# Kernel tuning notes

Measured on AMD Instinct MI355X. Metric: run time of the kernel, lower is better.

Reference implementation:

```python
import jax, jax.numpy as jnp
import numpy as np

BIG = 1e30  # stand-in for +inf that keeps gradients finite


def setup_inputs() -> dict:
    key = jax.random.key(0)
    B, D, N = 32, 128, 2048
    kx, ky, kl = jax.random.split(key, 3)
    x = jax.random.normal(kx, (B, D, N), dtype=jnp.float32)
    y = jax.random.normal(ky, (B, D, N), dtype=jnp.float32)
    # ragged cardinalities in [N//2, N]; every set nonempty
    lens = jax.random.randint(kl, (B,), N // 2, N + 1)
    mask = jnp.arange(N)[None, :] < lens[:, None]  # [B, N] bool
    return {"x": x, "y": y, "mask": mask}


def reference(x, y, mask):
    # x, y: [B, D, N]; mask: [B, N] bool (shared between x and y, as in original)
    xt = jnp.transpose(x, (0, 2, 1))  # [B, N, D]
    yt = jnp.transpose(y, (0, 2, 1))  # [B, N, D]
    x2 = jnp.sum(xt * xt, axis=-1)    # [B, N]
    y2 = jnp.sum(yt * yt, axis=-1)    # [B, N]
    # pairwise squared L2: [B, N, N], d[b,i,j] = ||x_i - y_j||^2
    d = x2[:, :, None] + y2[:, None, :] - 2.0 * jnp.einsum("bid,bjd->bij", xt, yt)
    m = mask
    # x_dist: for each valid y_j, min over valid x_i; then sum over valid j
    d_row = jnp.where(m[:, :, None], d, BIG)              # mask invalid i
    x_dist = jnp.sum(jnp.where(m, jnp.min(d_row, axis=1), 0.0), axis=1)  # [B]
    # y_dist: for each valid x_i, min over valid y_j; then sum over valid i
    d_col = jnp.where(m[:, None, :], d, BIG)              # mask invalid j
    y_dist = jnp.sum(jnp.where(m, jnp.min(d_col, axis=2), 0.0), axis=1)  # [B]
    return jnp.mean(x_dist + y_dist)
```

## Files before the change

### kernel.cpp

```cpp
#include <hip/hip_runtime.h>
#include <hip/hip_bf16.h>

#define BATCH 32
#define DIM   128
#define NPTS  2048
#define BIGF  1e30f

#define OFF_XT   0ull
#define OFF_YT   16777216ull
#define OFF_XN   33554432ull
#define OFF_YN   (33554432ull + 262144ull)
#define OFF_RMIN (33554432ull + 2ull * 262144ull)
#define OFF_CMIN (33554432ull + 3ull * 262144ull)

typedef __bf16 bf16x8 __attribute__((ext_vector_type(8)));
typedef float  f32x16 __attribute__((ext_vector_type(16)));

#define ZERO16 {0.f,0.f,0.f,0.f,0.f,0.f,0.f,0.f,0.f,0.f,0.f,0.f,0.f,0.f,0.f,0.f}

__device__ __forceinline__ bool mask_is_i32(const void* m) {
  return ((const unsigned char*)m)[1] == 0;
}
__device__ __forceinline__ bool mask_at(const void* m, bool i32, int idx) {
  return i32 ? (((const int*)m)[idx] != 0) : (((const unsigned char*)m)[idx] != 0);
}

__global__ void chamfer_prep(const float* __restrict__ x, const float* __restrict__ y,
                             const void* __restrict__ mask, char* __restrict__ ws,
                             float* __restrict__ out) {
  __shared__ float buf[128 * 132];
  __shared__ float nrm_part[2][128];

  int blk = blockIdx.x;
  int arr = blk >> 9;
  int b   = (blk >> 4) & 31;
  int nt  = blk & 15;
  int n0  = nt << 7;
  int tid = threadIdx.x;

  const float* src = (arr ? y : x) + (size_t)b * DIM * NPTS;

#pragma unroll
  for (int k = 0; k < 16; ++k) {
    int idx = k * 256 + tid;
    int d = idx >> 5, c4 = idx & 31;
    float4 v = *(const float4*)(src + (size_t)d * NPTS + n0 + c4 * 4);
    *(float4*)&buf[d * 132 + c4 * 4] = v;
  }
  __syncthreads();

  int n = tid & 127, half = tid >> 7;
  char* img = ws + (arr ? OFF_YT : OFF_XT) + ((size_t)b * NPTS + n0 + n) * 256;
  float sq = 0.f;
#pragma unroll
  for (int cl = 0; cl < 8; ++cl) {
    unsigned short h[8];
#pragma unroll
    for (int q = 0; q < 8; ++q) {
      int d = half * 64 + cl * 8 + q;
      float v = buf[d * 132 + n];
      __hip_bfloat16 bv = __float2bfloat16(v);
      h[q] = *(unsigned short*)&bv;
      float vb = __bfloat162float(bv);
      sq = fmaf(vb, vb, sq);
    }
    uint4 pk;
    pk.x = h[0] | ((unsigned)h[1] << 16);
    pk.y = h[2] | ((unsigned)h[3] << 16);
    pk.z = h[4] | ((unsigned)h[5] << 16);
    pk.w = h[6] | ((unsigned)h[7] << 16);
    int cg = half * 8 + cl;
    *(uint4*)(img + ((cg ^ (n & 7)) << 4)) = pk;
  }
  nrm_part[half][n] = sq;
  __syncthreads();
  if (half == 0) {
    float tot = nrm_part[0][n] + nrm_part[1][n];
    int row = n0 + n;
    bool i32 = mask_is_i32(mask);
    bool valid = mask_at(mask, i32, b * NPTS + row);
    float* nrm = (float*)(ws + (arr ? OFF_YN : OFF_XN));
    nrm[b * NPTS + row] = valid ? tot : BIGF;
    if (arr) ((unsigned*)(ws + OFF_CMIN))[b * NPTS + row] = __float_as_uint(BIGF);
  }
  if (blk == 0 && tid == 0) out[0] = 0.f;
}

__global__ __launch_bounds__(512, 2)
void chamfer_dist(char* __restrict__ ws) {
  __shared__ unsigned short ys[2][128 * 128];
  __shared__ unsigned colmin_lds[NPTS];

  int blk = blockIdx.x;
  int b  = blk & 31;
  int it = blk >> 5;
  int i0 = it << 8;
  int tid  = threadIdx.x;
  int lane = tid & 63;
  int w    = tid >> 6;
  int qrow = w >> 1, qcol = w & 1;
  int la31 = lane & 31, la5 = lane >> 5;

  const char* xTb = ws + OFF_XT + (size_t)b * NPTS * 256;
  const char* yTb = ws + OFF_YT + (size_t)b * NPTS * 256;
  const float* xng = (const float*)(ws + OFF_XN) + b * NPTS;
  const float* yng = (const float*)(ws + OFF_YN) + b * NPTS;
  float*    rowming = (float*)(ws + OFF_RMIN) + b * NPTS;
  unsigned* colming = (unsigned*)(ws + OFF_CMIN) + b * NPTS;

#pragma unroll
  for (int k = 0; k < NPTS / 512; ++k)
    colmin_lds[k * 512 + tid] = __float_as_uint(BIGF);

  int r0 = i0 + qrow * 64 + la31;
  int swA = (la31 & 7) << 4;
  const char* xrow0 = xTb + (size_t)r0 * 256;
  const char* xrow1 = xrow0 + 32 * 256;
  bf16x8 Areg0[8], Areg1[8];
#pragma unroll
  for (int kc = 0; kc < 8; ++kc) {
    int dbs = (((kc * 2 + la5) << 4)) ^ swA;
    Areg0[kc] = *(const bf16x8*)(xrow0 + dbs);
    Areg1[kc] = *(const bf16x8*)(xrow1 + dbs);
  }

  float xnr[2][16];
#pragma unroll
  for (int fm = 0; fm < 2; ++fm)
#pragma unroll
    for (int r = 0; r < 16; ++r) {
      int row = qrow * 64 + fm * 32 + (r & 3) + ((r >> 2) << 3) + (la5 << 2);
      xnr[fm][r] = xng[i0 + row];
    }
  float rmin[2][16];
#pragma unroll
  for (int fm = 0; fm < 2; ++fm)
#pragma unroll
    for (int r = 0; r < 16; ++r) rmin[fm][r] = BIGF;

#pragma unroll
  for (int k = 0; k < 4; ++k) {
    int idx = k * 512 + tid;
    *(uint4*)((char*)ys[0] + idx * 16) = *(const uint4*)(yTb + (size_t)idx * 16);
  }
  __syncthreads();

  int sw = (la31 & 7) << 4;
  int pcol0 = (qcol * 64 + la31) * 256;
  int pcol1 = pcol0 + 32 * 256;

  for (int jt = 0; jt < 16; ++jt) {
    int cur = jt & 1;
    uint4 stg0, stg1, stg2, stg3;
    if (jt < 15) {
      const char* base = yTb + (size_t)(jt + 1) * 128 * 256;
      stg0 = *(const uint4*)(base + (size_t)(tid)        * 16);
      stg1 = *(const uint4*)(base + (size_t)(512  + tid) * 16);
      stg2 = *(const uint4*)(base + (size_t)(1024 + tid) * 16);
      stg3 = *(const uint4*)(base + (size_t)(1536 + tid) * 16);
    }
    int j0t = jt * 128 + qcol * 64;
    float ynr0 = yng[j0t + la31];
    float ynr1 = yng[j0t + 32 + la31];

    const char* ysb = (const char*)ys[cur];
    f32x16 acc00 = ZERO16, acc01 = ZERO16, acc10 = ZERO16, acc11 = ZERO16;
#pragma unroll
    for (int kc = 0; kc < 8; ++kc) {
      int dbs = ((kc * 2 + la5) << 4) ^ sw;
      bf16x8 b0 = *(const bf16x8*)(ysb + pcol0 + dbs);
      bf16x8 b1 = *(const bf16x8*)(ysb + pcol1 + dbs);
      acc00 = __builtin_amdgcn_mfma_f32_32x32x16_bf16(Areg0[kc], b0, acc00, 0, 0, 0);
      acc01 = __builtin_amdgcn_mfma_f32_32x32x16_bf16(Areg0[kc], b1, acc01, 0, 0, 0);
      acc10 = __builtin_amdgcn_mfma_f32_32x32x16_bf16(Areg1[kc], b0, acc10, 0, 0, 0);
      acc11 = __builtin_amdgcn_mfma_f32_32x32x16_bf16(Areg1[kc], b1, acc11, 0, 0, 0);
    }
    float cm0 = BIGF, cm1 = BIGF;
#pragma unroll
    for (int r = 0; r < 16; ++r) {
      float d;
      d = fmaxf(fmaf(-2.f, acc00[r], xnr[0][r] + ynr0), 0.f);
      rmin[0][r] = fminf(rmin[0][r], d); cm0 = fminf(cm0, d);
      d = fmaxf(fmaf(-2.f, acc01[r], xnr[0][r] + ynr1), 0.f);
      rmin[0][r] = fminf(rmin[0][r], d); cm1 = fminf(cm1, d);
      d = fmaxf(fmaf(-2.f, acc10[r], xnr[1][r] + ynr0), 0.f);
      rmin[1][r] = fminf(rmin[1][r], d); cm0 = fminf(cm0, d);
      d = fmaxf(fmaf(-2.f, acc11[r], xnr[1][r] + ynr1), 0.f);
      rmin[1][r] = fminf(rmin[1][r], d); cm1 = fminf(cm1, d);
    }
    cm0 = fminf(cm0, __shfl_xor(cm0, 32));
    cm1 = fminf(cm1, __shfl_xor(cm1, 32));
    if (lane < 32) {
      atomicMin(&colmin_lds[j0t + la31],      __float_as_uint(cm0));
      atomicMin(&colmin_lds[j0t + 32 + la31], __float_as_uint(cm1));
    }
    if (jt < 15) {
      char* dst = (char*)ys[cur ^ 1];
      *(uint4*)(dst + (size_t)(tid)        * 16) = stg0;
      *(uint4*)(dst + (size_t)(512  + tid) * 16) = stg1;
      *(uint4*)(dst + (size_t)(1024 + tid) * 16) = stg2;
      *(uint4*)(dst + (size_t)(1536 + tid) * 16) = stg3;
    }
    __syncthreads();
  }

  for (int idx = tid; idx < NPTS; idx += 512)
    atomicMin(&colming[idx], colmin_lds[idx]);

#pragma unroll
  for (int fm = 0; fm < 2; ++fm)
#pragma unroll
    for (int r = 0; r < 16; ++r) {
      float v = rmin[fm][r];
      v = fminf(v, __shfl_xor(v, 1));
      v = fminf(v, __shfl_xor(v, 2));
      v = fminf(v, __shfl_xor(v, 4));
      v = fminf(v, __shfl_xor(v, 8));
      v = fminf(v, __shfl_xor(v, 16));
      if (la31 == 0) {
        int row = qrow * 64 + fm * 32 + (r & 3) + ((r >> 2) << 3) + (la5 << 2);
        rowming[i0 + row] = v;
      }
    }
}

__global__ void chamfer_reduce(const char* __restrict__ ws, const void* __restrict__ mask,
                               float* __restrict__ out) {
  __shared__ float red[256];
  int b = blockIdx.x;
  int tid = threadIdx.x;
  bool i32 = mask_is_i32(mask);
  const float*    rowmin = (const float*)(ws + OFF_RMIN) + b * NPTS;
  const unsigned* colmin = (const unsigned*)(ws + OFF_CMIN) + b * NPTS;
  float s = 0.f;
  for (int i = tid; i < NPTS; i += 256) {
    if (mask_at(mask, i32, b * NPTS + i))
      s += rowmin[i] + __uint_as_float(colmin[i]);
  }
  red[tid] = s;
  __syncthreads();
  for (int st = 128; st > 0; st >>= 1) {
    if (tid < st) red[tid] += red[tid + st];
    __syncthreads();
  }
  if (tid == 0) atomicAdd(out, red[0] * (1.f / BATCH));
}

extern "C" void kernel_launch(void* const* d_in, const int* in_sizes, int n_in,
                              void* d_out, int out_size, void* d_ws, size_t ws_size,
                              hipStream_t stream) {
  const float* x = (const float*)d_in[0];
  const float* y = (const float*)d_in[1];
  const void* mask = d_in[2];
  float* out = (float*)d_out;
  char* ws = (char*)d_ws;

  chamfer_prep<<<1024, 256, 0, stream>>>(x, y, mask, ws, out);
  chamfer_dist<<<256, 512, 0, stream>>>(ws);
  chamfer_reduce<<<32, 256, 0, stream>>>(ws, mask, out);
}
```

Baseline: 159.2 us.

## Skip masked tiles, use direct global-to-LDS loads with new bf16 layout

Prep blocks whose first point is masked out now just write sentinel norms, and dist blocks compute the valid length and skip row tiles past it. They also limit column tiles to that length. The bf16 workspace layout changes from swizzled row-major to chunk-major, and Y tiles (256 columns) are staged with global_load_lds async copies instead of register staging. The distance epilogue moves the x-norm add out of the row-min loop, and reduce uses four times as many blocks. Occupancy drops to one block per CU (larger LDS). The chunk-major LDS reads may hit bank conflicts now that the XOR swizzle is gone.

```diff
diff --git a/kernel.cpp b/kernel.cpp
--- a/kernel.cpp
+++ b/kernel.cpp
@@ -4,17 +4,19 @@
 #define BATCH 32
 #define DIM   128
 #define NPTS  2048
+#define NCH   16
 #define BIGF  1e30f
 
 #define OFF_XT   0ull
 #define OFF_YT   16777216ull
 #define OFF_XN   33554432ull
-#define OFF_YN   (33554432ull + 262144ull)
-#define OFF_RMIN (33554432ull + 2ull * 262144ull)
-#define OFF_CMIN (33554432ull + 3ull * 262144ull)
+#define OFF_YN   (OFF_XN + 262144ull)
+#define OFF_RMIN (OFF_XN + 2ull * 262144ull)
+#define OFF_CMIN (OFF_XN + 3ull * 262144ull)
 
 typedef __bf16 bf16x8 __attribute__((ext_vector_type(8)));
 typedef float  f32x16 __attribute__((ext_vector_type(16)));
+typedef unsigned int u32;
 
 #define ZERO16 {0.f,0.f,0.f,0.f,0.f,0.f,0.f,0.f,0.f,0.f,0.f,0.f,0.f,0.f,0.f,0.f}
 
@@ -23,6 +25,12 @@
 }
 __device__ __forceinline__ bool mask_at(const void* m, bool i32, int idx) {
   return i32 ? (((const int*)m)[idx] != 0) : (((const unsigned char*)m)[idx] != 0);
+}
+
+__device__ __forceinline__ void gll16(const void* g, void* l) {
+  __builtin_amdgcn_global_load_lds(
+      (const __attribute__((address_space(1))) u32*)g,
+      (__attribute__((address_space(3))) u32*)l, 16, 0, 0);
 }
 
 __global__ void chamfer_prep(const float* __restrict__ x, const float* __restrict__ y,
@@ -37,28 +45,40 @@
   int nt  = blk & 15;
   int n0  = nt << 7;
   int tid = threadIdx.x;
+  bool i32m = mask_is_i32(mask);
+
+  if (blk == 0 && tid == 0) out[0] = 0.f;
+
+  float*    nrm  = (float*)(ws + (arr ? OFF_YN : OFF_XN));
+  unsigned* cmin = (unsigned*)(ws + OFF_CMIN);
+
+  if (!mask_at(mask, i32m, b * NPTS + n0)) {
+    if (tid < 128) {
+      nrm[b * NPTS + n0 + tid] = BIGF;
+      if (arr) cmin[b * NPTS + n0 + tid] = __float_as_uint(BIGF);
+    }
+    return;
+  }
 
   const float* src = (arr ? y : x) + (size_t)b * DIM * NPTS;
-
 #pragma unroll
   for (int k = 0; k < 16; ++k) {
     int idx = k * 256 + tid;
     int d = idx >> 5, c4 = idx & 31;
-    float4 v = *(const float4*)(src + (size_t)d * NPTS + n0 + c4 * 4);
-    *(float4*)&buf[d * 132 + c4 * 4] = v;
+    *(float4*)&buf[d * 132 + c4 * 4] =
+        *(const float4*)(src + (size_t)d * NPTS + n0 + c4 * 4);
   }
   __syncthreads();
 
   int n = tid & 127, half = tid >> 7;
-  char* img = ws + (arr ? OFF_YT : OFF_XT) + ((size_t)b * NPTS + n0 + n) * 256;
+  char* imgbase = ws + (arr ? OFF_YT : OFF_XT);
   float sq = 0.f;
 #pragma unroll
   for (int cl = 0; cl < 8; ++cl) {
     unsigned short h[8];
 #pragma unroll
     for (int q = 0; q < 8; ++q) {
-      int d = half * 64 + cl * 8 + q;
-      float v = buf[d * 132 + n];
+      float v = buf[(half * 64 + cl * 8 + q) * 132 + n];
       __hip_bfloat16 bv = __float2bfloat16(v);
       h[q] = *(unsigned short*)&bv;
       float vb = __bfloat162float(bv);
@@ -70,141 +90,141 @@
     pk.z = h[4] | ((unsigned)h[5] << 16);
     pk.w = h[6] | ((unsigned)h[7] << 16);
     int cg = half * 8 + cl;
-    *(uint4*)(img + ((cg ^ (n & 7)) << 4)) = pk;
+    *(uint4*)(imgbase + (((size_t)(b * NCH + cg) * NPTS + n0 + n) << 4)) = pk;
   }
   nrm_part[half][n] = sq;
   __syncthreads();
   if (half == 0) {
     float tot = nrm_part[0][n] + nrm_part[1][n];
     int row = n0 + n;
-    bool i32 = mask_is_i32(mask);
-    bool valid = mask_at(mask, i32, b * NPTS + row);
-    float* nrm = (float*)(ws + (arr ? OFF_YN : OFF_XN));
+    bool valid = mask_at(mask, i32m, b * NPTS + row);
     nrm[b * NPTS + row] = valid ? tot : BIGF;
-    if (arr) ((unsigned*)(ws + OFF_CMIN))[b * NPTS + row] = __float_as_uint(BIGF);
-  }
-  if (blk == 0 && tid == 0) out[0] = 0.f;
-}
-
-__global__ __launch_bounds__(512, 2)
-void chamfer_dist(char* __restrict__ ws) {
-  __shared__ unsigned short ys[2][128 * 128];
+    if (arr) cmin[b * NPTS + row] = __float_as_uint(BIGF);
+  }
+}
+
+__global__ __launch_bounds__(512, 1)
+void chamfer_dist(char* __restrict__ ws, const void* __restrict__ mask) {
+  __shared__ __align__(16) char ysl[2][NCH * 256 * 16];
   __shared__ unsigned colmin_lds[NPTS];
+  __shared__ int lred[8];
 
   int blk = blockIdx.x;
   int b  = blk & 31;
   int it = blk >> 5;
   int i0 = it << 8;
-  int tid  = threadIdx.x;
-  int lane = tid & 63;
-  int w    = tid >> 6;
-  int qrow = w >> 1, qcol = w & 1;
-  int la31 = lane & 31, la5 = lane >> 5;
-
-  const char* xTb = ws + OFF_XT + (size_t)b * NPTS * 256;
-  const char* yTb = ws + OFF_YT + (size_t)b * NPTS * 256;
+  int tid = threadIdx.x, lane = tid & 63, w = tid >> 6;
+  int qrow = w >> 1, qcol = w & 1, la31 = lane & 31, la5 = lane >> 5;
+
+  bool i32m = mask_is_i32(mask);
+  int cnt = 0;
+#pragma unroll
+  for (int k = 0; k < 4; ++k)
+    cnt += mask_at(mask, i32m, b * NPTS + k * 512 + tid) ? 1 : 0;
+#pragma unroll
+  for (int s = 1; s < 64; s <<= 1) cnt += __shfl_xor(cnt, s);
+  if (lane == 0) lred[w] = cnt;
+  __syncthreads();
+  int len = 0;
+#pragma unroll
+  for (int k = 0; k < 8; ++k) len += lred[k];
+  if (i0 >= len) return;
+
+  const char* xTb = ws + OFF_XT + ((size_t)b * NCH * NPTS << 4);
+  const char* yTb = ws + OFF_YT + ((size_t)b * NCH * NPTS << 4);
   const float* xng = (const float*)(ws + OFF_XN) + b * NPTS;
   const float* yng = (const float*)(ws + OFF_YN) + b * NPTS;
   float*    rowming = (float*)(ws + OFF_RMIN) + b * NPTS;
   unsigned* colming = (unsigned*)(ws + OFF_CMIN) + b * NPTS;
 
 #pragma unroll
-  for (int k = 0; k < NPTS / 512; ++k)
+  for (int k = 0; k < 4; ++k)
     colmin_lds[k * 512 + tid] = __float_as_uint(BIGF);
 
   int r0 = i0 + qrow * 64 + la31;
-  int swA = (la31 & 7) << 4;
-  const char* xrow0 = xTb + (size_t)r0 * 256;
-  const char* xrow1 = xrow0 + 32 * 256;
   bf16x8 Areg0[8], Areg1[8];
 #pragma unroll
   for (int kc = 0; kc < 8; ++kc) {
-    int dbs = (((kc * 2 + la5) << 4)) ^ swA;
-    Areg0[kc] = *(const bf16x8*)(xrow0 + dbs);
-    Areg1[kc] = *(const bf16x8*)(xrow1 + dbs);
-  }
-
-  float xnr[2][16];
+    int c = kc * 2 + la5;
+    Areg0[kc] = *(const bf16x8*)(xTb + (((size_t)c * NPTS + r0) << 4));
+    Areg1[kc] = *(const bf16x8*)(xTb + (((size_t)c * NPTS + r0 + 32) << 4));
+  }
+
+  float xnr[2][16], rmin[2][16];
 #pragma unroll
   for (int fm = 0; fm < 2; ++fm)
 #pragma unroll
     for (int r = 0; r < 16; ++r) {
       int row = qrow * 64 + fm * 32 + (r & 3) + ((r >> 2) << 3) + (la5 << 2);
       xnr[fm][r] = xng[i0 + row];
-    }
-  float rmin[2][16];
-#pragma unroll
-  for (int fm = 0; fm < 2; ++fm)
-#pragma unroll
-    for (int r = 0; r < 16; ++r) rmin[fm][r] = BIGF;
-
-#pragma unroll
-  for (int k = 0; k < 4; ++k) {
+      rmin[fm][r] = BIGF;
+    }
+
+  int nT = (len + 255) >> 8;
+
+#pragma unroll
+  for (int k = 0; k < 8; ++k) {
     int idx = k * 512 + tid;
-    *(uint4*)((char*)ys[0] + idx * 16) = *(const uint4*)(yTb + (size_t)idx * 16);
-  }
-  __syncthreads();
-
-  int sw = (la31 & 7) << 4;
-  int pcol0 = (qcol * 64 + la31) * 256;
-  int pcol1 = pcol0 + 32 * 256;
-
-  for (int jt = 0; jt < 16; ++jt) {
-    int cur = jt & 1;
-    uint4 stg0, stg1, stg2, stg3;
-    if (jt < 15) {
-      const char* base = yTb + (size_t)(jt + 1) * 128 * 256;
-      stg0 = *(const uint4*)(base + (size_t)(tid)        * 16);
-      stg1 = *(const uint4*)(base + (size_t)(512  + tid) * 16);
-      stg2 = *(const uint4*)(base + (size_t)(1024 + tid) * 16);
-      stg3 = *(const uint4*)(base + (size_t)(1536 + tid) * 16);
-    }
-    int j0t = jt * 128 + qcol * 64;
-    float ynr0 = yng[j0t + la31];
-    float ynr1 = yng[j0t + 32 + la31];
-
-    const char* ysb = (const char*)ys[cur];
-    f32x16 acc00 = ZERO16, acc01 = ZERO16, acc10 = ZERO16, acc11 = ZERO16;
-#pragma unroll
-    for (int kc = 0; kc < 8; ++kc) {
-      int dbs = ((kc * 2 + la5) << 4) ^ sw;
-      bf16x8 b0 = *(const bf16x8*)(ysb + pcol0 + dbs);
-      bf16x8 b1 = *(const bf16x8*)(ysb + pcol1 + dbs);
-      acc00 = __builtin_amdgcn_mfma_f32_32x32x16_bf16(Areg0[kc], b0, acc00, 0, 0, 0);
-      acc01 = __builtin_amdgcn_mfma_f32_32x32x16_bf16(Areg0[kc], b1, acc01, 0, 0, 0);
-      acc10 = __builtin_amdgcn_mfma_f32_32x32x16_bf16(Areg1[kc], b0, acc10, 0, 0, 0);
-      acc11 = __builtin_amdgcn_mfma_f32_32x32x16_bf16(Areg1[kc], b1, acc11, 0, 0, 0);
-    }
-    float cm0 = BIGF, cm1 = BIGF;
-#pragma unroll
-    for (int r = 0; r < 16; ++r) {
-      float d;
-      d = fmaxf(fmaf(-2.f, acc00[r], xnr[0][r] + ynr0), 0.f);
-      rmin[0][r] = fminf(rmin[0][r], d); cm0 = fminf(cm0, d);
-      d = fmaxf(fmaf(-2.f, acc01[r], xnr[0][r] + ynr1), 0.f);
-      rmin[0][r] = fminf(rmin[0][r], d); cm1 = fminf(cm1, d);
-      d = fmaxf(fmaf(-2.f, acc10[r], xnr[1][r] + ynr0), 0.f);
-      rmin[1][r] = fminf(rmin[1][r], d); cm0 = fminf(cm0, d);
-      d = fmaxf(fmaf(-2.f, acc11[r], xnr[1][r] + ynr1), 0.f);
-      rmin[1][r] = fminf(rmin[1][r], d); cm1 = fminf(cm1, d);
-    }
-    cm0 = fminf(cm0, __shfl_xor(cm0, 32));
-    cm1 = fminf(cm1, __shfl_xor(cm1, 32));
-    if (lane < 32) {
-      atomicMin(&colmin_lds[j0t + la31],      __float_as_uint(cm0));
-      atomicMin(&colmin_lds[j0t + 32 + la31], __float_as_uint(cm1));
-    }
-    if (jt < 15) {
-      char* dst = (char*)ys[cur ^ 1];
-      *(uint4*)(dst + (size_t)(tid)        * 16) = stg0;
-      *(uint4*)(dst + (size_t)(512  + tid) * 16) = stg1;
-      *(uint4*)(dst + (size_t)(1024 + tid) * 16) = stg2;
-      *(uint4*)(dst + (size_t)(1536 + tid) * 16) = stg3;
+    gll16(yTb + (((size_t)(idx >> 8) * NPTS + (idx & 255)) << 4),
+          &ysl[0][idx * 16]);
+  }
+  __syncthreads();
+
+  for (int t = 0; t < nT; ++t) {
+    int cur = t & 1;
+    if (t + 1 < nT) {
+      int j0n = (t + 1) << 8;
+#pragma unroll
+      for (int k = 0; k < 8; ++k) {
+        int idx = k * 512 + tid;
+        gll16(yTb + (((size_t)(idx >> 8) * NPTS + j0n + (idx & 255)) << 4),
+              &ysl[cur ^ 1][idx * 16]);
+      }
+    }
+    const char* ybuf = (const char*)ysl[cur];
+#pragma unroll
+    for (int sub = 0; sub < 2; ++sub) {
+      int jbase = (sub << 7) + qcol * 64;
+      int j0t = (t << 8) + jbase;
+      float ynr0 = yng[j0t + la31];
+      float ynr1 = yng[j0t + 32 + la31];
+
+      f32x16 acc00 = ZERO16, acc01 = ZERO16, acc10 = ZERO16, acc11 = ZERO16;
+#pragma unroll
+      for (int kc = 0; kc < 8; ++kc) {
+        int c = kc * 2 + la5;
+        int boff = (c * 256 + jbase + la31) << 4;
+        bf16x8 b0 = *(const bf16x8*)(ybuf + boff);
+        bf16x8 b1 = *(const bf16x8*)(ybuf + boff + (32 << 4));
+        acc00 = __builtin_amdgcn_mfma_f32_32x32x16_bf16(Areg0[kc], b0, acc00, 0, 0, 0);
+        acc01 = __builtin_amdgcn_mfma_f32_32x32x16_bf16(Areg0[kc], b1, acc01, 0, 0, 0);
+        acc10 = __builtin_amdgcn_mfma_f32_32x32x16_bf16(Areg1[kc], b0, acc10, 0, 0, 0);
+        acc11 = __builtin_amdgcn_mfma_f32_32x32x16_bf16(Areg1[kc], b1, acc11, 0, 0, 0);
+      }
+      float cm0 = BIGF, cm1 = BIGF;
+#pragma unroll
+      for (int r = 0; r < 16; ++r) {
+        float u00 = fmaf(-2.f, acc00[r], ynr0);
+        float u01 = fmaf(-2.f, acc01[r], ynr1);
+        float u10 = fmaf(-2.f, acc10[r], ynr0);
+        float u11 = fmaf(-2.f, acc11[r], ynr1);
+        rmin[0][r] = fminf(rmin[0][r], fminf(u00, u01));
+        rmin[1][r] = fminf(rmin[1][r], fminf(u10, u11));
+        cm0 = fminf(cm0, fminf(u00 + xnr[0][r], u10 + xnr[1][r]));
+        cm1 = fminf(cm1, fminf(u01 + xnr[0][r], u11 + xnr[1][r]));
+      }
+      cm0 = fminf(cm0, __shfl_xor(cm0, 32));
+      cm1 = fminf(cm1, __shfl_xor(cm1, 32));
+      if (lane < 32) {
+        atomicMin(&colmin_lds[j0t + la31],      __float_as_uint(fmaxf(cm0, 0.f)));
+        atomicMin(&colmin_lds[j0t + 32 + la31], __float_as_uint(fmaxf(cm1, 0.f)));
+      }
     }
     __syncthreads();
   }
 
-  for (int idx = tid; idx < NPTS; idx += 512)
+  int jmax = nT << 8; if (jmax > NPTS) jmax = NPTS;
+  for (int idx = tid; idx < jmax; idx += 512)
     atomicMin(&colming[idx], colmin_lds[idx]);
 
 #pragma unroll
@@ -219,7 +239,7 @@
       v = fminf(v, __shfl_xor(v, 16));
       if (la31 == 0) {
         int row = qrow * 64 + fm * 32 + (r & 3) + ((r >> 2) << 3) + (la5 << 2);
-        rowming[i0 + row] = v;
+        rowming[i0 + row] = fmaxf(v + xnr[fm][r], 0.f);
       }
     }
 }
@@ -227,14 +247,17 @@
 __global__ void chamfer_reduce(const char* __restrict__ ws, const void* __restrict__ mask,
                                float* __restrict__ out) {
   __shared__ float red[256];
-  int b = blockIdx.x;
+  int blk = blockIdx.x;
+  int b = blk >> 2, sl = blk & 3;
   int tid = threadIdx.x;
-  bool i32 = mask_is_i32(mask);
+  bool i32m = mask_is_i32(mask);
   const float*    rowmin = (const float*)(ws + OFF_RMIN) + b * NPTS;
   const unsigned* colmin = (const unsigned*)(ws + OFF_CMIN) + b * NPTS;
   float s = 0.f;
-  for (int i = tid; i < NPTS; i += 256) {
-    if (mask_at(mask, i32, b * NPTS + i))
+#pragma unroll
+  for (int k = 0; k < 2; ++k) {
+    int i = sl * 512 + k * 256 + tid;
+    if (mask_at(mask, i32m, b * NPTS + i))
       s += rowmin[i] + __uint_as_float(colmin[i]);
   }
   red[tid] = s;
@@ -256,6 +279,6 @@
   char* ws = (char*)d_ws;
 
   chamfer_prep<<<1024, 256, 0, stream>>>(x, y, mask, ws, out);
-  chamfer_dist<<<256, 512, 0, stream>>>(ws);
-  chamfer_reduce<<<32, 256, 0, stream>>>(ws, mask, out);
-}
+  chamfer_dist<<<256, 512, 0, stream>>>(ws, mask);
+  chamfer_reduce<<<128, 256, 0, stream>>>(ws, mask, out);
+}
```

Result: slower. 193.3 us (+21.5%).
